# Kernel optimization log

Measured on AMD Instinct MI355X. Metric: run time of the kernel, lower is better.

The kernel has to match this reference:

```python
import jax, jax.numpy as jnp
import numpy as np

B, S_SRC, S_TRG = 128, 512, 128
VIN, VOUT = 128, 128
E, H = 128, 256          # embed, encoder hidden
HD = 2 * H               # decoder hidden = 512 (concat of bi-dir encoder states)
DENC = 2 * H             # encoder output feature dim = 512


def setup_inputs() -> dict:
    key = jax.random.key(0)
    ks = jax.random.split(key, 20)
    g = lambda k, shape: (jax.random.normal(k, shape, jnp.float32) * 0.05)
    inp = {
        "src": jax.random.randint(ks[0], (B, S_SRC), 0, VIN, jnp.int32),
        "trg": jax.random.randint(ks[1], (B, S_TRG), 0, VOUT, jnp.int32),
        # encoder
        "enc_emb": g(ks[2], (VIN, E)),
        "enc_Wih_f": g(ks[3], (4 * H, E)),
        "enc_Whh_f": g(ks[4], (4 * H, H)),
        "enc_b_f": g(ks[5], (4 * H,)),
        "enc_Wih_b": g(ks[6], (4 * H, E)),
        "enc_Whh_b": g(ks[7], (4 * H, H)),
        "enc_b_b": g(ks[8], (4 * H,)),
        # decoder
        "dec_emb": g(ks[9], (VOUT, E)),
        "dec_Wih": g(ks[10], (4 * HD, E + DENC)),
        "dec_Whh": g(ks[11], (4 * HD, HD)),
        "dec_b": g(ks[12], (4 * HD,)),
        # attention: Linear(dec_hid + enc_dim -> HD), v: Linear(HD -> 1)
        "attn_W": g(ks[13], (HD + DENC, HD)),
        "attn_b": g(ks[14], (HD,)),
        "attn_v": g(ks[15], (HD,)),
        # output projection
        "out_W": g(ks[16], (HD, VOUT)),
        "out_b": g(ks[17], (VOUT,)),
    }
    return inp


def _lstm_cell(h, c, x, Wih, Whh, b):
    gates = x @ Wih.T + h @ Whh.T + b               # [B, 4H]
    i, f, gg, o = jnp.split(gates, 4, axis=-1)       # PyTorch gate order i,f,g,o
    i, f, o = jax.nn.sigmoid(i), jax.nn.sigmoid(f), jax.nn.sigmoid(o)
    c = f * c + i * jnp.tanh(gg)
    h = o * jnp.tanh(c)
    return h, c


def _lstm_scan(xs, Wih, Whh, b, reverse=False):
    # xs: [S, B, E] -> hs: [S, B, H] (time-aligned), plus final (h, c)
    Bn, Hn = xs.shape[1], Whh.shape[1]
    init = (jnp.zeros((Bn, Hn), xs.dtype), jnp.zeros((Bn, Hn), xs.dtype))
    def step(carry, x):
        h, c = _lstm_cell(carry[0], carry[1], x, Wih, Whh, b)
        return (h, c), h
    (h, c), hs = jax.lax.scan(step, init, xs, reverse=reverse)
    return hs, h, c


def reference(src, trg, enc_emb, enc_Wih_f, enc_Whh_f, enc_b_f,
              enc_Wih_b, enc_Whh_b, enc_b_b, dec_emb, dec_Wih, dec_Whh,
              dec_b, attn_W, attn_b, attn_v, out_W, out_b):
    # ----- encoder (bidirectional LSTM) -----
    emb = enc_emb[src]                                # [B, S, E]
    xs = jnp.swapaxes(emb, 0, 1)                      # [S, B, E]
    hs_f, hf, cf = _lstm_scan(xs, enc_Wih_f, enc_Whh_f, enc_b_f, reverse=False)
    hs_b, hb, cb = _lstm_scan(xs, enc_Wih_b, enc_Whh_b, enc_b_b, reverse=True)
    enc_out = jnp.swapaxes(jnp.concatenate([hs_f, hs_b], -1), 0, 1)  # [B, S, 2H]
    hidden = jnp.concatenate([hf, hb], -1)            # [B, HD]  (hidden.view(1,B,-1))
    cell = jnp.concatenate([cf, cb], -1)              # [B, HD]

    # attention linear split: energy = tanh([h, enc] @ W + b)
    Wh, We = attn_W[:HD], attn_W[HD:]
    enc_proj = jnp.einsum("bsd,de->bse", enc_out, We)  # [B, S, HD] precomputed

    def dec_step(carry, tok):
        h, c = carry
        e = jnp.tanh(h[:, None, :] @ Wh + enc_proj + attn_b)     # [B, S, HD]
        scores = jnp.einsum("bse,e->bs", e, attn_v)              # [B, S]
        aw = jax.nn.softmax(scores, axis=1)
        ctx = jnp.einsum("bs,bsd->bd", aw, enc_out)              # [B, DENC]
        x = jnp.concatenate([dec_emb[tok], ctx], -1)             # [B, E+DENC]
        h, c = _lstm_cell(h, c, x, dec_Wih, dec_Whh, dec_b)
        logits = h @ out_W + out_b                               # [B, VOUT]
        return (h, c), logits

    # teacher forcing (ratio=1.0): input at step t is trg[:, t-1], t = 1..T-1
    toks = jnp.swapaxes(trg[:, :-1], 0, 1)            # [T-1, B]
    _, logits = jax.lax.scan(dec_step, (hidden, cell), toks)
    logits = jnp.swapaxes(logits, 0, 1)               # [B, T-1, VOUT]
    outputs = jnp.concatenate(
        [jnp.zeros((src.shape[0], 1, VOUT), logits.dtype), logits], axis=1)
    return outputs
```

## Files before the change

kernel.cpp:

```cpp
#include <hip/hip_runtime.h>


typedef _Float16 f16;
typedef _Float16 half8 __attribute__((ext_vector_type(8)));
typedef float f32x4 __attribute__((ext_vector_type(4)));
typedef char char8v __attribute__((ext_vector_type(8)));

#define MFMA16(a, b, c) __builtin_amdgcn_mfma_f32_16x16x32_f16((a), (b), (c), 0, 0, 0)

#define PSCALE (2.5f / 127.f)
#define PINV   (127.f / 2.5f)

__device__ __forceinline__ float fsig(float x) {
    return __builtin_amdgcn_rcpf(1.f + __expf(-x));
}
__device__ __forceinline__ float ftanh(float x) {
    return 1.f - 2.f * __builtin_amdgcn_rcpf(1.f + __expf(2.f * x));
}
__device__ __forceinline__ int frag_idx(int m, int k, int KS) {
    return (((m >> 4) * KS + (k >> 5)) * 64 + (((k >> 3) & 3) * 16 + (m & 15))) * 8 + (k & 7);
}

__device__ __forceinline__ void lds_barrier() {
    asm volatile("s_waitcnt lgkmcnt(0)" ::: "memory");
    __builtin_amdgcn_sched_barrier(0);
    __builtin_amdgcn_s_barrier();
    __builtin_amdgcn_sched_barrier(0);
}

__global__ void k_zero(unsigned* __restrict__ s)
{
    for (int z = threadIdx.x; z < 4112; z += 256) s[z] = 0u;
}

__global__ __launch_bounds__(256) void k_prep(
    const float* __restrict__ attn_W, const float* __restrict__ out_W,
    const float* __restrict__ enc_emb,
    const float* __restrict__ wihf, const float* __restrict__ wihb,
    const float* __restrict__ whhf, const float* __restrict__ whhb,
    const float* __restrict__ dec_emb, const float* __restrict__ dec_wih,
    const float* __restrict__ dec_whh,
    f16* __restrict__ WhT_sw, f16* __restrict__ outWT_sw,
    f16* __restrict__ whhf_sw, f16* __restrict__ whhb_sw,
    f16* __restrict__ decwih_sw, f16* __restrict__ decwhh_sw,
    f16* __restrict__ WeT, f16* __restrict__ emb16,
    f16* __restrict__ wihf16, f16* __restrict__ wihb16,
    f16* __restrict__ decemb16, float* __restrict__ out)
{
    long i = (long)blockIdx.x * 256 + threadIdx.x;
    if (i >= 3784704L) return;
    long idx = i;
    if (idx < 262144) {
        int j = idx & 7, lane = (idx >> 3) & 63, c = lane & 15, q = lane >> 4;
        int ks = (idx >> 9) & 15, nt = idx >> 13;
        WhT_sw[idx] = (f16)attn_W[(ks * 32 + q * 8 + j) * 512 + nt * 16 + c];
        return;
    }
    idx -= 262144;
    if (idx < 65536) {
        int j = idx & 7, lane = (idx >> 3) & 63, c = lane & 15, q = lane >> 4;
        int ks = (idx >> 9) & 15, nt = idx >> 13;
        outWT_sw[idx] = (f16)out_W[(ks * 32 + q * 8 + j) * 128 + nt * 16 + c];
        return;
    }
    idx -= 65536;
    if (idx < 262144) {
        int j = idx & 7, lane = (idx >> 3) & 63, c = lane & 15, q = lane >> 4;
        int ks = (idx >> 9) & 7, nt = idx >> 12;
        whhf_sw[idx] = (f16)whhf[(nt * 16 + c) * 256 + ks * 32 + q * 8 + j];
        return;
    }
    idx -= 262144;
    if (idx < 262144) {
        int j = idx & 7, lane = (idx >> 3) & 63, c = lane & 15, q = lane >> 4;
        int ks = (idx >> 9) & 7, nt = idx >> 12;
        whhb_sw[idx] = (f16)whhb[(nt * 16 + c) * 256 + ks * 32 + q * 8 + j];
        return;
    }
    idx -= 262144;
    if (idx < 1310720) {
        int j = idx & 7, lane = (idx >> 3) & 63, c = lane & 15, q = lane >> 4;
        int r2 = idx >> 9; int ks = r2 % 20, nt = r2 / 20;
        decwih_sw[idx] = (f16)dec_wih[(nt * 16 + c) * 640 + ks * 32 + q * 8 + j];
        return;
    }
    idx -= 1310720;
    if (idx < 1048576) {
        int j = idx & 7, lane = (idx >> 3) & 63, c = lane & 15, q = lane >> 4;
        int ks = (idx >> 9) & 15, nt = idx >> 13;
        decwhh_sw[idx] = (f16)dec_whh[(nt * 16 + c) * 512 + ks * 32 + q * 8 + j];
        return;
    }
    idx -= 1048576;
    if (idx < 262144) { int e = idx >> 9, d = idx & 511; WeT[idx] = (f16)attn_W[(512 + d) * 512 + e]; return; }
    idx -= 262144;
    if (idx < 16384)  { emb16[idx] = (f16)enc_emb[idx]; return; }
    idx -= 16384;
    if (idx < 131072) { wihf16[idx] = (f16)wihf[idx]; return; }
    idx -= 131072;
    if (idx < 131072) { wihb16[idx] = (f16)wihb[idx]; return; }
    idx -= 131072;
    if (idx < 16384)  { decemb16[idx] = (f16)dec_emb[idx]; return; }
    idx -= 16384;
    if (idx < 16384)  { int b = idx >> 7, v = idx & 127; out[b * 16384 + v] = 0.f; return; }
}

__global__ __launch_bounds__(256) void k_vocab(
    const f16* __restrict__ emb, const f16* __restrict__ wihf,
    const f16* __restrict__ wihb, const float* __restrict__ bf_,
    const float* __restrict__ bb_, f16* __restrict__ xg_vocab)
{
    int bn = blockIdx.x;
    int tid = threadIdx.x, wave = tid >> 6, lane = tid & 63;
    int col = lane & 15, quad = lane >> 4;
    int wr = wave >> 1, wc = wave & 1;

    f32x4 acc[4][4] = {};
    for (int ks = 0; ks < 4; ++ks) {
        int k0 = ks * 32 + quad * 8;
        half8 a[4], bfr[4];
        for (int i = 0; i < 4; ++i)
            a[i] = *(const half8*)(emb + (wr * 64 + i * 16 + col) * 128 + k0);
        for (int j = 0; j < 4; ++j) {
            int n = bn * 128 + wc * 64 + j * 16 + col;
            const f16* wp = (n < 1024) ? (wihf + n * 128) : (wihb + (n - 1024) * 128);
            bfr[j] = *(const half8*)(wp + k0);
        }
        for (int i = 0; i < 4; ++i)
            for (int j = 0; j < 4; ++j)
                acc[i][j] = MFMA16(a[i], bfr[j], acc[i][j]);
    }
    for (int j = 0; j < 4; ++j) {
        int n = bn * 128 + wc * 64 + j * 16 + col;
        float bias = (n < 1024) ? bf_[n] : bb_[n - 1024];
        for (int i = 0; i < 4; ++i) {
            int vbase = wr * 64 + i * 16 + quad * 4;
            for (int r = 0; r < 4; ++r)
                xg_vocab[(vbase + r) * 2048 + n] = (f16)(acc[i][j][r] + bias);
        }
    }
}

__global__ __launch_bounds__(512, 1) void k_enc(
    const int* __restrict__ src, const f16* __restrict__ xg_vocab,
    const f16* __restrict__ whhf_sw, const f16* __restrict__ whhb_sw,
    f16* __restrict__ enc_out, f16* __restrict__ hdec0, float* __restrict__ c_ws)
{
    int blk = blockIdx.x;
    int dir = blk >> 3, bbase = (blk & 7) * 16;
    int tid = threadIdx.x, wave = tid >> 6, lane = tid & 63;
    int col = lane & 15, quad = lane >> 4;
    const f16* whh = dir ? whhb_sw : whhf_sw;

    __shared__ f16 hb[2][16][264];
    __shared__ f16 xvb[2][16][1032];
    __shared__ unsigned short stall[8192];

    for (int z = tid; z < 2 * 16 * 264; z += 512) ((f16*)hb)[z] = (f16)0.f;
    for (int z = tid; z < 8192; z += 512) stall[z] = (unsigned short)src[bbase * 512 + z];
    float cc[2][4] = {};

    half8 bst[16];
    #pragma unroll
    for (int nt = 0; nt < 2; ++nt)
        #pragma unroll
        for (int kk = 0; kk < 8; ++kk) {
            int tile = wave * 2 + nt;
            bst[nt * 8 + kk] = *(const half8*)(whh + ((tile * 8 + kk) * 64 + lane) * 8);
        }
    __syncthreads();

    int xrow = tid >> 7, xoff = (tid & 127) * 8;
    half8 xr[4];
    {
        int ts0 = dir ? 511 : 0;
        #pragma unroll
        for (int it = 0; it < 4; ++it) {
            int row = it * 4 + xrow;
            int tok = stall[row * 512 + ts0];
            xr[it] = *(const half8*)(xg_vocab + tok * 2048 + dir * 1024 + xoff);
        }
        #pragma unroll
        for (int it = 0; it < 4; ++it)
            *(half8*)(&xvb[0][it * 4 + xrow][xoff]) = xr[it];
    }
    __syncthreads();

    int ts_prev = 0;
    for (int t = 0; t < 512; ++t) {
        int ts = dir ? (511 - t) : t;
        int cur = t & 1, prv = cur ^ 1;

        if (t < 511) {
            int tsn = dir ? (510 - t) : (t + 1);
            #pragma unroll
            for (int it = 0; it < 4; ++it) {
                int row = it * 4 + xrow;
                int tok = stall[row * 512 + tsn];
                xr[it] = *(const half8*)(xg_vocab + tok * 2048 + dir * 1024 + xoff);
            }
        }

        if (t > 0) {
            int b = tid >> 5, seg = tid & 31;
            *(half8*)(enc_out + ((size_t)(bbase + b) * 512 + ts_prev) * 512 + dir * 256 + seg * 8) =
                *(const half8*)(&hb[prv][b][seg * 8]);
        }

        half8 a[8];
        #pragma unroll
        for (int kk = 0; kk < 8; ++kk)
            a[kk] = *(const half8*)(&hb[prv][col][kk * 32 + quad * 8]);

        f32x4 acc[4][2] = {};
        #pragma unroll
        for (int kk = 0; kk < 8; ++kk) {
            half8 bv[6];
            #pragma unroll
            for (int g = 1; g < 4; ++g)
                #pragma unroll
                for (int nt = 0; nt < 2; ++nt) {
                    int tile = g * 16 + wave * 2 + nt;
                    bv[(g - 1) * 2 + nt] =
                        *(const half8*)(whh + ((tile * 8 + kk) * 64 + lane) * 8);
                }
            #pragma unroll
            for (int nt = 0; nt < 2; ++nt)
                acc[0][nt] = MFMA16(a[kk], bst[nt * 8 + kk], acc[0][nt]);
            #pragma unroll
            for (int g = 1; g < 4; ++g)
                #pragma unroll
                for (int nt = 0; nt < 2; ++nt)
                    acc[g][nt] = MFMA16(a[kk], bv[(g - 1) * 2 + nt], acc[g][nt]);
        }

        #pragma unroll
        for (int nt = 0; nt < 2; ++nt) {
            int hcol = wave * 32 + nt * 16 + col;
            #pragma unroll
            for (int r = 0; r < 4; ++r) {
                int b = quad * 4 + r;
                float gi = (float)xvb[cur][b][0 * 256 + hcol] + acc[0][nt][r];
                float gf = (float)xvb[cur][b][1 * 256 + hcol] + acc[1][nt][r];
                float gg = (float)xvb[cur][b][2 * 256 + hcol] + acc[2][nt][r];
                float go = (float)xvb[cur][b][3 * 256 + hcol] + acc[3][nt][r];
                float ig = fsig(gi), fg = fsig(gf), g2 = ftanh(gg), og = fsig(go);
                float cv = fg * cc[nt][r] + ig * g2;
                cc[nt][r] = cv;
                float h = og * ftanh(cv);
                hb[cur][b][hcol] = (f16)h;
            }
        }

        if (t < 511) {
            #pragma unroll
            for (int it = 0; it < 4; ++it)
                *(half8*)(&xvb[prv][it * 4 + xrow][xoff]) = xr[it];
        }

        lds_barrier();
        ts_prev = ts;
    }

    {
        int b = tid >> 5, seg = tid & 31;
        *(half8*)(enc_out + ((size_t)(bbase + b) * 512 + ts_prev) * 512 + dir * 256 + seg * 8) =
            *(const half8*)(&hb[1][b][seg * 8]);
    }
    #pragma unroll
    for (int nt = 0; nt < 2; ++nt) {
        int hcol = wave * 32 + nt * 16 + col;
        #pragma unroll
        for (int r = 0; r < 4; ++r) {
            int b = quad * 4 + r;
            int m = bbase + b, k = dir * 256 + hcol;
            hdec0[frag_idx(m, k, 16)] = hb[1][b][hcol];
            c_ws[m * 512 + k] = cc[nt][r];
        }
    }
}

__global__ __launch_bounds__(256) void k_proj(
    const f16* __restrict__ enc_out, const f16* __restrict__ WeT,
    char* __restrict__ proj8)
{
    int blk = blockIdx.x;
    int bm = blk & 511, bn = blk >> 9;
    int tid = threadIdx.x, wave = tid >> 6, lane = tid & 63;
    int col = lane & 15, quad = lane >> 4;
    int wr = wave >> 1, wc = wave & 1;

    f32x4 acc[4][4] = {};
    for (int ks = 0; ks < 16; ++ks) {
        int k0 = ks * 32 + quad * 8;
        half8 a[4], bfr[4];
        for (int i = 0; i < 4; ++i) {
            int m = bm * 128 + wr * 64 + i * 16 + col;
            a[i] = *(const half8*)(enc_out + (size_t)m * 512 + k0);
        }
        for (int j = 0; j < 4; ++j) {
            int n = bn * 128 + wc * 64 + j * 16 + col;
            bfr[j] = *(const half8*)(WeT + n * 512 + k0);
        }
        for (int i = 0; i < 4; ++i)
            for (int j = 0; j < 4; ++j)
                acc[i][j] = MFMA16(a[i], bfr[j], acc[i][j]);
    }
    for (int j = 0; j < 4; ++j) {
        int n = bn * 128 + wc * 64 + j * 16 + col;
        for (int i = 0; i < 4; ++i) {
            int mbase = bm * 128 + wr * 64 + i * 16 + quad * 4;
            for (int r = 0; r < 4; ++r) {
                float v = acc[i][j][r] * PINV;
                int q = (int)rintf(v);
                q = (q > 127) ? 127 : ((q < -127) ? -127 : q);
                proj8[(size_t)(mbase + r) * 512 + n] = (char)q;
            }
        }
    }
}

__global__ __launch_bounds__(256) void k_qinit(
    const f16* __restrict__ h0_sw, const f16* __restrict__ WhT_sw,
    float* __restrict__ qpart)
{
    int j = blockIdx.x;
    int tid = threadIdx.x, wave = tid >> 6, lane = tid & 63;
    int col = lane & 15, quad = lane >> 4;
    half8 a[2];
    #pragma unroll
    for (int i = 0; i < 2; ++i)
        a[i] = *(const half8*)(h0_sw + (((wave * 2 + i) * 16 + j) * 64 + lane) * 8);
    for (int nt = 0; nt < 32; ++nt) {
        half8 bfr = *(const half8*)(WhT_sw + ((nt * 16 + j) * 64 + lane) * 8);
        f32x4 q0 = {}, q1 = {};
        q0 = MFMA16(a[0], bfr, q0);
        q1 = MFMA16(a[1], bfr, q1);
        #pragma unroll
        for (int r = 0; r < 4; ++r) {
            qpart[(j * 128 + wave * 32 + quad * 4 + r) * 512 + nt * 16 + col] = q0[r];
            qpart[(j * 128 + wave * 32 + 16 + quad * 4 + r) * 512 + nt * 16 + col] = q1[r];
        }
    }
}

__global__ __launch_bounds__(512, 4) void k_step(
    const char* __restrict__ proj8, const f16* __restrict__ enc_out,
    float* __restrict__ qpart, const float* __restrict__ attn_bp,
    const float* __restrict__ attn_vp, const int* __restrict__ trg,
    const f16* __restrict__ dec_emb, f16* __restrict__ x_sw,
    float* __restrict__ part_m, float* __restrict__ part_l,
    float* __restrict__ part_ctx, f16* __restrict__ hdec0,
    f16* __restrict__ hdec1, const f16* __restrict__ wih_sw,
    const f16* __restrict__ whh_sw, const float* __restrict__ dec_bp,
    float* __restrict__ c_ws, f16* __restrict__ hhist_sw,
    const f16* __restrict__ WhT_sw, unsigned* __restrict__ flags, int tt)
{
    int blk = blockIdx.x;
    int tid = threadIdx.x, wave = tid >> 6, lane = tid & 63;
    int col = lane & 15, quad = lane >> 4;

    __shared__ float q[512];
    __shared__ float sc[256];
    __shared__ float ctxred[8][512];
    __shared__ float wred[8], wred2[8];
    __shared__ f16 hsl[64][40];
    __shared__ float gm[64][2];
    __shared__ int islast;

    if (blk < 32) {
        int tg = tt - 1;
        if (tg >= 0) {
            int j = blk >> 1, mh = blk & 1;
            if (tid < 64) {
                int bb = mh * 64 + tid;
                float m0 = part_m[bb * 2 + 0], m1 = part_m[bb * 2 + 1];
                float l0 = part_l[bb * 2 + 0], l1 = part_l[bb * 2 + 1];
                float M = fmaxf(m0, m1);
                float g0 = __expf(m0 - M), g1 = __expf(m1 - M);
                float inv = 1.f / (g0 * l0 + g1 * l1);
                gm[tid][0] = g0 * inv;
                gm[tid][1] = g1 * inv;
            }
            __syncthreads();
            for (int z = tid; z < 32768; z += 512) {
                int lr = z >> 9, d = z & 511;
                int bb = mh * 64 + lr;
                float c = gm[lr][0] * part_ctx[(size_t)(bb * 2 + 0) * 512 + d]
                        + gm[lr][1] * part_ctx[(size_t)(bb * 2 + 1) * 512 + d];
                x_sw[frag_idx(bb, 128 + d, 20)] = (f16)c;
            }
            __syncthreads();

            if (tid < 256) {
                const f16* hprev = (tg & 1) ? hdec1 : hdec0;
                f16* hnext = (tg & 1) ? hdec0 : hdec1;

                f32x4 acc[8] = {};
                for (int ks = 0; ks < 36; ++ks) {
                    int mtile = mh * 4 + wave;
                    half8 a = (ks < 20)
                        ? *(const half8*)(x_sw + ((mtile * 20 + ks) * 64 + lane) * 8)
                        : *(const half8*)(hprev + ((mtile * 16 + (ks - 20)) * 64 + lane) * 8);
                    half8 bv[8];
                    #pragma unroll
                    for (int jt = 0; jt < 8; ++jt) {
                        int g = jt >> 1, u2 = jt & 1;
                        int ntile = g * 32 + j * 2 + u2;
                        bv[jt] = (ks < 20)
                            ? *(const half8*)(wih_sw + ((ntile * 20 + ks) * 64 + lane) * 8)
                            : *(const half8*)(whh_sw + ((ntile * 16 + (ks - 20)) * 64 + lane) * 8);
                    }
                    #pragma unroll
                    for (int jt = 0; jt < 8; ++jt)
                        acc[jt] = MFMA16(a, bv[jt], acc[jt]);
                }
                float bias[8];
                #pragma unroll
                for (int jt = 0; jt < 8; ++jt) {
                    int g = jt >> 1, u2 = jt & 1;
                    bias[jt] = dec_bp[g * 512 + j * 32 + u2 * 16 + col];
                }
                #pragma unroll
                for (int r = 0; r < 4; ++r) {
                    int lb = wave * 16 + quad * 4 + r;
                    int bb = mh * 64 + lb;
                    #pragma unroll
                    for (int u2 = 0; u2 < 2; ++u2) {
                        int hl = u2 * 16 + col, hcol = j * 32 + hl;
                        float gi = acc[0 + u2][r] + bias[0 + u2];
                        float gf = acc[2 + u2][r] + bias[2 + u2];
                        float gg = acc[4 + u2][r] + bias[4 + u2];
                        float go = acc[6 + u2][r] + bias[6 + u2];
                        float ig = fsig(gi), fg = fsig(gf), g2 = ftanh(gg), og = fsig(go);
                        float cv = fg * c_ws[bb * 512 + hcol] + ig * g2;
                        c_ws[bb * 512 + hcol] = cv;
                        float h = og * ftanh(cv);
                        f16 h16 = (f16)h;
                        int fidx = frag_idx(bb, hcol, 16);
                        hnext[fidx] = h16;
                        hhist_sw[tg * 65536 + fidx] = h16;
                        hsl[lb][hl] = h16;
                    }
                }
                half8 aq = *(const half8*)(&hsl[wave * 16 + col][quad * 8]);
                for (int nt = 0; nt < 32; ++nt) {
                    half8 bq = *(const half8*)(WhT_sw + ((nt * 16 + j) * 64 + lane) * 8);
                    f32x4 q0 = {};
                    q0 = MFMA16(aq, bq, q0);
                    #pragma unroll
                    for (int r = 0; r < 4; ++r)
                        qpart[(j * 128 + mh * 64 + wave * 16 + quad * 4 + r) * 512 + nt * 16 + col] = q0[r];
                }
            }

            __syncthreads();
            if (tid == 0) {
                unsigned old = __hip_atomic_fetch_add(flags, 1u, __ATOMIC_ACQ_REL,
                                                      __HIP_MEMORY_SCOPE_AGENT);
                islast = (old == (unsigned)(32 * tt - 1)) ? 1 : 0;
            }
            __syncthreads();
            if (islast && tid < 256)
                __hip_atomic_store(flags + 16 + tid * 16, (unsigned)tt,
                                   __ATOMIC_RELEASE, __HIP_MEMORY_SCOPE_AGENT);
        }
        return;
    }

    int ab = blk - 32;
    int b = ab >> 1, sh = ab & 1;
    int sbase = sh * 256;

    float vreg[8];
    #pragma unroll
    for (int u = 0; u < 8; ++u) vreg[u] = attn_vp[lane * 8 + u];
    float abias = attn_bp[tid];

    if (tt > 0) {
        if (tid == 0) {
            while (__hip_atomic_load(flags + 16 + ab * 16, __ATOMIC_RELAXED,
                                     __HIP_MEMORY_SCOPE_AGENT) < (unsigned)tt)
                __builtin_amdgcn_s_sleep(16);
            (void)__hip_atomic_load(flags + 16 + ab * 16, __ATOMIC_ACQUIRE,
                                    __HIP_MEMORY_SCOPE_AGENT);
        }
        __syncthreads();
    }

    {
        float s = abias;
        #pragma unroll
        for (int jj = 0; jj < 16; ++jj) s += qpart[(jj * 128 + b) * 512 + tid];
        q[tid] = s;
    }
    __syncthreads();

    float qreg[8];
    #pragma unroll
    for (int u = 0; u < 8; ++u) qreg[u] = q[lane * 8 + u];

    for (int ib = 0; ib < 4; ++ib) {
        char8v p[8];
        #pragma unroll
        for (int z = 0; z < 8; ++z) {
            int sl = (ib * 8 + z) * 8 + wave;
            p[z] = *(const char8v*)(proj8 + ((size_t)b * 512 + sbase + sl) * 512 + lane * 8);
        }
        #pragma unroll
        for (int z = 0; z < 8; ++z) {
            int sl = (ib * 8 + z) * 8 + wave;
            float part = 0.f;
            #pragma unroll
            for (int u = 0; u < 8; ++u)
                part += vreg[u] * ftanh(fmaf((float)p[z][u], PSCALE, qreg[u]));
            #pragma unroll
            for (int o = 32; o; o >>= 1) part += __shfl_xor(part, o);
            if (lane == 0) sc[sl] = part;
        }
    }
    __syncthreads();

    float s0 = (tid < 256) ? sc[tid] : -__builtin_inff();
    float mv = s0;
    #pragma unroll
    for (int o = 32; o; o >>= 1) mv = fmaxf(mv, __shfl_xor(mv, o));
    if (lane == 0) wred[wave] = mv;
    __syncthreads();
    float M = wred[0];
    #pragma unroll
    for (int w = 1; w < 8; ++w) M = fmaxf(M, wred[w]);
    float e0 = (tid < 256) ? __expf(s0 - M) : 0.f;
    if (tid < 256) sc[tid] = e0;
    float sm = e0;
    #pragma unroll
    for (int o = 32; o; o >>= 1) sm += __shfl_xor(sm, o);
    if (lane == 0) wred2[wave] = sm;
    __syncthreads();
    float lsum = wred2[0];
    #pragma unroll
    for (int w = 1; w < 8; ++w) lsum += wred2[w];

    float a8[8] = {};
    for (int ib = 0; ib < 4; ++ib) {
        half8 ev[8];
        float wgt[8];
        #pragma unroll
        for (int z = 0; z < 8; ++z) {
            int sl = (ib * 8 + z) * 8 + wave;
            ev[z] = *(const half8*)(enc_out + ((size_t)b * 512 + sbase + sl) * 512 + lane * 8);
            wgt[z] = sc[sl];
        }
        #pragma unroll
        for (int z = 0; z < 8; ++z)
            #pragma unroll
            for (int u = 0; u < 8; ++u) a8[u] += wgt[z] * (float)ev[z][u];
    }
    #pragma unroll
    for (int u = 0; u < 8; ++u) ctxred[wave][lane * 8 + u] = a8[u];
    __syncthreads();
    float cp = 0.f;
    #pragma unroll
    for (int w = 0; w < 8; ++w) cp += ctxred[w][tid];
    part_ctx[(size_t)ab * 512 + tid] = cp;
    if (tid == 0) { part_m[ab] = M; part_l[ab] = lsum; }

    if (sh == 0 && tid < 128) {
        int tok = trg[b * 128 + tt];
        x_sw[frag_idx(b, tid, 20)] = dec_emb[tok * 128 + tid];
    }
}

__global__ __launch_bounds__(256) void k_gates(
    f16* __restrict__ x_sw, const f16* __restrict__ hprev_sw,
    const f16* __restrict__ wih_sw, const f16* __restrict__ whh_sw,
    const float* __restrict__ dec_b, float* __restrict__ c_ws,
    f16* __restrict__ hnext_sw, f16* __restrict__ hhist_sw,
    const f16* __restrict__ WhT_sw, float* __restrict__ qpart,
    const float* __restrict__ part_m, const float* __restrict__ part_l,
    const float* __restrict__ part_ctx, int t)
{
    int jb = blockIdx.x;
    int j = jb >> 1, mh = jb & 1;
    int tid = threadIdx.x, wave = tid >> 6, lane = tid & 63;
    int col = lane & 15, quad = lane >> 4;
    __shared__ f16 hsl[64][40];
    __shared__ float gm[64][2];

    if (tid < 64) {
        int bb = mh * 64 + tid;
        float m0 = part_m[bb * 2 + 0], m1 = part_m[bb * 2 + 1];
        float l0 = part_l[bb * 2 + 0], l1 = part_l[bb * 2 + 1];
        float M = fmaxf(m0, m1);
        float g0 = __expf(m0 - M), g1 = __expf(m1 - M);
        float inv = 1.f / (g0 * l0 + g1 * l1);
        gm[tid][0] = g0 * inv;
        gm[tid][1] = g1 * inv;
    }
    __syncthreads();
    for (int z = tid; z < 32768; z += 256) {
        int lr = z >> 9, d = z & 511;
        int bb = mh * 64 + lr;
        float c = gm[lr][0] * part_ctx[(size_t)(bb * 2 + 0) * 512 + d]
                + gm[lr][1] * part_ctx[(size_t)(bb * 2 + 1) * 512 + d];
        x_sw[frag_idx(bb, 128 + d, 20)] = (f16)c;
    }
    __syncthreads();

    f32x4 acc[8] = {};
    for (int ks = 0; ks < 36; ++ks) {
        int mtile = mh * 4 + wave;
        half8 a = (ks < 20)
            ? *(const half8*)(x_sw + ((mtile * 20 + ks) * 64 + lane) * 8)
            : *(const half8*)(hprev_sw + ((mtile * 16 + (ks - 20)) * 64 + lane) * 8);
        half8 bv[8];
        #pragma unroll
        for (int jt = 0; jt < 8; ++jt) {
            int g = jt >> 1, u2 = jt & 1;
            int ntile = g * 32 + j * 2 + u2;
            bv[jt] = (ks < 20)
                ? *(const half8*)(wih_sw + ((ntile * 20 + ks) * 64 + lane) * 8)
                : *(const half8*)(whh_sw + ((ntile * 16 + (ks - 20)) * 64 + lane) * 8);
        }
        #pragma unroll
        for (int jt = 0; jt < 8; ++jt)
            acc[jt] = MFMA16(a, bv[jt], acc[jt]);
    }
    float bias[8];
    #pragma unroll
    for (int jt = 0; jt < 8; ++jt) {
        int g = jt >> 1, u2 = jt & 1;
        bias[jt] = dec_b[g * 512 + j * 32 + u2 * 16 + col];
    }
    #pragma unroll
    for (int r = 0; r < 4; ++r) {
        int lb = wave * 16 + quad * 4 + r;
        int bb = mh * 64 + lb;
        #pragma unroll
        for (int u2 = 0; u2 < 2; ++u2) {
            int hl = u2 * 16 + col, hcol = j * 32 + hl;
            float gi = acc[0 + u2][r] + bias[0 + u2];
            float gf = acc[2 + u2][r] + bias[2 + u2];
            float gg = acc[4 + u2][r] + bias[4 + u2];
            float go = acc[6 + u2][r] + bias[6 + u2];
            float ig = fsig(gi), fg = fsig(gf), g2 = ftanh(gg), og = fsig(go);
            float cv = fg * c_ws[bb * 512 + hcol] + ig * g2;
            c_ws[bb * 512 + hcol] = cv;
            float h = og * ftanh(cv);
            f16 h16 = (f16)h;
            int fidx = frag_idx(bb, hcol, 16);
            hnext_sw[fidx] = h16;
            hhist_sw[t * 65536 + fidx] = h16;
            hsl[lb][hl] = h16;
        }
    }
    half8 aq = *(const half8*)(&hsl[wave * 16 + col][quad * 8]);
    for (int nt = 0; nt < 32; ++nt) {
        half8 bq = *(const half8*)(WhT_sw + ((nt * 16 + j) * 64 + lane) * 8);
        f32x4 q0 = {};
        q0 = MFMA16(aq, bq, q0);
        #pragma unroll
        for (int r = 0; r < 4; ++r)
            qpart[(j * 128 + mh * 64 + wave * 16 + quad * 4 + r) * 512 + nt * 16 + col] = q0[r];
    }
}

__global__ __launch_bounds__(256) void k_logits(
    const f16* __restrict__ hhist_sw, const f16* __restrict__ outWT_sw,
    const float* __restrict__ out_b, float* __restrict__ out)
{
    int bt = blockIdx.x;
    int tid = threadIdx.x, wave = tid >> 6, lane = tid & 63;
    int col = lane & 15, quad = lane >> 4;
    f32x4 acc[2][8] = {};
    for (int ks = 0; ks < 16; ++ks) {
        half8 a[2];
        #pragma unroll
        for (int i = 0; i < 2; ++i)
            a[i] = *(const half8*)(hhist_sw + bt * 65536 + (((wave * 2 + i) * 16 + ks) * 64 + lane) * 8);
        half8 bv[8];
        #pragma unroll
        for (int jt = 0; jt < 8; ++jt)
            bv[jt] = *(const half8*)(outWT_sw + ((jt * 16 + ks) * 64 + lane) * 8);
        #pragma unroll
        for (int jt = 0; jt < 8; ++jt) {
            acc[0][jt] = MFMA16(a[0], bv[jt], acc[0][jt]);
            acc[1][jt] = MFMA16(a[1], bv[jt], acc[1][jt]);
        }
    }
    #pragma unroll
    for (int jt = 0; jt < 8; ++jt) {
        float bias = out_b[jt * 16 + col];
        #pragma unroll
        for (int i = 0; i < 2; ++i)
            #pragma unroll
            for (int r = 0; r < 4; ++r) {
                int br = wave * 32 + i * 16 + quad * 4 + r;
                out[br * 16384 + (bt + 1) * 128 + jt * 16 + col] = acc[i][jt][r] + bias;
            }
    }
}

extern "C" void kernel_launch(void* const* d_in, const int* in_sizes, int n_in,
                              void* d_out, int out_size, void* d_ws, size_t ws_size,
                              hipStream_t stream)
{
    (void)in_sizes; (void)n_in; (void)out_size;
    if (ws_size < 130000000) return;

    const int*   src     = (const int*)d_in[0];
    const int*   trg     = (const int*)d_in[1];
    const float* enc_emb = (const float*)d_in[2];
    const float* wihf    = (const float*)d_in[3];
    const float* whhf    = (const float*)d_in[4];
    const float* bf_     = (const float*)d_in[5];
    const float* wihb    = (const float*)d_in[6];
    const float* whhb    = (const float*)d_in[7];
    const float* bb_     = (const float*)d_in[8];
    const float* dec_emb = (const float*)d_in[9];
    const float* dec_wih = (const float*)d_in[10];
    const float* dec_whh = (const float*)d_in[11];
    const float* dec_b   = (const float*)d_in[12];
    const float* attn_W  = (const float*)d_in[13];
    const float* attn_b  = (const float*)d_in[14];
    const float* attn_v  = (const float*)d_in[15];
    const float* out_W   = (const float*)d_in[16];
    const float* out_b   = (const float*)d_in[17];
    float* out = (float*)d_out;

    char* p = (char*)d_ws;
    auto carve = [&](size_t n) { char* r = p; p += ((n + 255) & ~(size_t)255); return r; };
    f16*   enc_out   = (f16*)  carve(67108864);
    char*  proj8     = (char*) carve(33554432);
    f16*   WhT_sw    = (f16*)  carve(524288);
    f16*   WeT       = (f16*)  carve(524288);
    f16*   outWT_sw  = (f16*)  carve(131072);
    f16*   emb16     = (f16*)  carve(32768);
    f16*   wihf16    = (f16*)  carve(262144);
    f16*   wihb16    = (f16*)  carve(262144);
    f16*   whhf_sw   = (f16*)  carve(524288);
    f16*   whhb_sw   = (f16*)  carve(524288);
    f16*   decemb16  = (f16*)  carve(32768);
    f16*   decwih_sw = (f16*)  carve(2621440);
    f16*   decwhh_sw = (f16*)  carve(2097152);
    float* qpart     = (float*)carve(4194304);
    f16*   hdec0     = (f16*)  carve(131072);
    f16*   hdec1     = (f16*)  carve(131072);
    float* c_ws      = (float*)carve(262144);
    f16*   x_sw      = (f16*)  carve(163840);
    f16*   hhist_sw  = (f16*)  carve(16646144);
    f16*   xg_vocab  = (f16*)  carve(524288);
    float* part_m    = (float*)carve(2048);
    float* part_l    = (float*)carve(2048);
    float* part_ctx  = (float*)carve(524288);
    unsigned* flagsv = (unsigned*)carve(16448);

    k_zero<<<1, 256, 0, stream>>>(flagsv);
    k_prep<<<14784, 256, 0, stream>>>(attn_W, out_W, enc_emb, wihf, wihb, whhf, whhb,
                                      dec_emb, dec_wih, dec_whh,
                                      WhT_sw, outWT_sw, whhf_sw, whhb_sw,
                                      decwih_sw, decwhh_sw, WeT, emb16,
                                      wihf16, wihb16, decemb16, out);
    k_vocab<<<16, 256, 0, stream>>>(emb16, wihf16, wihb16, bf_, bb_, xg_vocab);
    k_enc<<<16, 512, 0, stream>>>(src, xg_vocab, whhf_sw, whhb_sw, enc_out, hdec0, c_ws);
    k_proj<<<2048, 256, 0, stream>>>(enc_out, WeT, proj8);
    k_qinit<<<16, 256, 0, stream>>>(hdec0, WhT_sw, qpart);

    for (int tt = 0; tt < 127; ++tt)
        k_step<<<288, 512, 0, stream>>>(proj8, enc_out, qpart, attn_b, attn_v,
                                        trg, decemb16, x_sw, part_m, part_l,
                                        part_ctx, hdec0, hdec1, decwih_sw,
                                        decwhh_sw, dec_b, c_ws, hhist_sw,
                                        WhT_sw, flagsv, tt);
    k_gates<<<32, 256, 0, stream>>>(x_sw, hdec0, decwih_sw, decwhh_sw, dec_b,
                                    c_ws, hdec1, hhist_sw, WhT_sw, qpart,
                                    part_m, part_l, part_ctx, 126);

    k_logits<<<127, 256, 0, stream>>>(hhist_sw, outWT_sw, out_b, out);
}
```

Baseline: 12.46 ms.

## Use one 1024-thread attention block per batch row, dropping split-softmax merge

Attention blocks now cover all 512 source positions of one batch row with 1024 threads, instead of two 512-thread blocks each covering half the sequence. The full softmax and context are finished inside one block and written straight into x_sw. This removes the partial max/sum/context buffers and the merge pass the gate blocks used to run before their GEMM. The final gates kernel is cut down to skip the unused q projection and hidden write. In exchange there are half as many attention blocks, each with more threads and shared memory, so occupancy and per-step latency may shift.

```diff
diff --git a/kernel.cpp b/kernel.cpp
--- a/kernel.cpp
+++ b/kernel.cpp
@@ -344,54 +344,32 @@
     }
 }
 
-__global__ __launch_bounds__(512, 4) void k_step(
+__global__ __launch_bounds__(1024, 4) void k_step(
     const char* __restrict__ proj8, const f16* __restrict__ enc_out,
     float* __restrict__ qpart, const float* __restrict__ attn_bp,
     const float* __restrict__ attn_vp, const int* __restrict__ trg,
     const f16* __restrict__ dec_emb, f16* __restrict__ x_sw,
-    float* __restrict__ part_m, float* __restrict__ part_l,
-    float* __restrict__ part_ctx, f16* __restrict__ hdec0,
-    f16* __restrict__ hdec1, const f16* __restrict__ wih_sw,
-    const f16* __restrict__ whh_sw, const float* __restrict__ dec_bp,
-    float* __restrict__ c_ws, f16* __restrict__ hhist_sw,
-    const f16* __restrict__ WhT_sw, unsigned* __restrict__ flags, int tt)
+    f16* __restrict__ hdec0, f16* __restrict__ hdec1,
+    const f16* __restrict__ wih_sw, const f16* __restrict__ whh_sw,
+    const float* __restrict__ dec_bp, float* __restrict__ c_ws,
+    f16* __restrict__ hhist_sw, const f16* __restrict__ WhT_sw,
+    unsigned* __restrict__ flags, int tt)
 {
     int blk = blockIdx.x;
     int tid = threadIdx.x, wave = tid >> 6, lane = tid & 63;
     int col = lane & 15, quad = lane >> 4;
 
     __shared__ float q[512];
-    __shared__ float sc[256];
-    __shared__ float ctxred[8][512];
-    __shared__ float wred[8], wred2[8];
+    __shared__ float sc[512];
+    __shared__ float ctxred[16][512];
+    __shared__ float wred[16], wred2[16];
     __shared__ f16 hsl[64][40];
-    __shared__ float gm[64][2];
     __shared__ int islast;
 
     if (blk < 32) {
         int tg = tt - 1;
         if (tg >= 0) {
             int j = blk >> 1, mh = blk & 1;
-            if (tid < 64) {
-                int bb = mh * 64 + tid;
-                float m0 = part_m[bb * 2 + 0], m1 = part_m[bb * 2 + 1];
-                float l0 = part_l[bb * 2 + 0], l1 = part_l[bb * 2 + 1];
-                float M = fmaxf(m0, m1);
-                float g0 = __expf(m0 - M), g1 = __expf(m1 - M);
-                float inv = 1.f / (g0 * l0 + g1 * l1);
-                gm[tid][0] = g0 * inv;
-                gm[tid][1] = g1 * inv;
-            }
-            __syncthreads();
-            for (int z = tid; z < 32768; z += 512) {
-                int lr = z >> 9, d = z & 511;
-                int bb = mh * 64 + lr;
-                float c = gm[lr][0] * part_ctx[(size_t)(bb * 2 + 0) * 512 + d]
-                        + gm[lr][1] * part_ctx[(size_t)(bb * 2 + 1) * 512 + d];
-                x_sw[frag_idx(bb, 128 + d, 20)] = (f16)c;
-            }
-            __syncthreads();
-
             if (tid < 256) {
                 const f16* hprev = (tg & 1) ? hdec1 : hdec0;
                 f16* hnext = (tg & 1) ? hdec0 : hdec1;
@@ -461,35 +439,32 @@
                 islast = (old == (unsigned)(32 * tt - 1)) ? 1 : 0;
             }
             __syncthreads();
-            if (islast && tid < 256)
+            if (islast && tid < 128)
                 __hip_atomic_store(flags + 16 + tid * 16, (unsigned)tt,
                                    __ATOMIC_RELEASE, __HIP_MEMORY_SCOPE_AGENT);
         }
         return;
     }
 
-    int ab = blk - 32;
-    int b = ab >> 1, sh = ab & 1;
-    int sbase = sh * 256;
+    int b = blk - 32;
 
     float vreg[8];
     #pragma unroll
     for (int u = 0; u < 8; ++u) vreg[u] = attn_vp[lane * 8 + u];
-    float abias = attn_bp[tid];
 
     if (tt > 0) {
         if (tid == 0) {
-            while (__hip_atomic_load(flags + 16 + ab * 16, __ATOMIC_RELAXED,
+            while (__hip_atomic_load(flags + 16 + b * 16, __ATOMIC_RELAXED,
                                      __HIP_MEMORY_SCOPE_AGENT) < (unsigned)tt)
                 __builtin_amdgcn_s_sleep(16);
-            (void)__hip_atomic_load(flags + 16 + ab * 16, __ATOMIC_ACQUIRE,
+            (void)__hip_atomic_load(flags + 16 + b * 16, __ATOMIC_ACQUIRE,
                                     __HIP_MEMORY_SCOPE_AGENT);
         }
         __syncthreads();
     }
 
-    {
-        float s = abias;
+    if (tid < 512) {
+        float s = attn_bp[tid];
         #pragma unroll
         for (int jj = 0; jj < 16; ++jj) s += qpart[(jj * 128 + b) * 512 + tid];
         q[tid] = s;
@@ -504,12 +479,12 @@
         char8v p[8];
         #pragma unroll
         for (int z = 0; z < 8; ++z) {
-            int sl = (ib * 8 + z) * 8 + wave;
-            p[z] = *(const char8v*)(proj8 + ((size_t)b * 512 + sbase + sl) * 512 + lane * 8);
+            int sl = (ib * 8 + z) * 16 + wave;
+            p[z] = *(const char8v*)(proj8 + ((size_t)b * 512 + sl) * 512 + lane * 8);
         }
         #pragma unroll
         for (int z = 0; z < 8; ++z) {
-            int sl = (ib * 8 + z) * 8 + wave;
+            int sl = (ib * 8 + z) * 16 + wave;
             float part = 0.f;
             #pragma unroll
             for (int u = 0; u < 8; ++u)
@@ -521,7 +496,7 @@
     }
     __syncthreads();
 
-    float s0 = (tid < 256) ? sc[tid] : -__builtin_inff();
+    float s0 = (tid < 512) ? sc[tid] : -__builtin_inff();
     float mv = s0;
     #pragma unroll
     for (int o = 32; o; o >>= 1) mv = fmaxf(mv, __shfl_xor(mv, o));
@@ -529,9 +504,9 @@
     __syncthreads();
     float M = wred[0];
     #pragma unroll
-    for (int w = 1; w < 8; ++w) M = fmaxf(M, wred[w]);
-    float e0 = (tid < 256) ? __expf(s0 - M) : 0.f;
-    if (tid < 256) sc[tid] = e0;
+    for (int w = 1; w < 16; ++w) M = fmaxf(M, wred[w]);
+    float e0 = (tid < 512) ? __expf(s0 - M) : 0.f;
+    if (tid < 512) sc[tid] = e0;
     float sm = e0;
     #pragma unroll
     for (int o = 32; o; o >>= 1) sm += __shfl_xor(sm, o);
@@ -539,7 +514,7 @@
     __syncthreads();
     float lsum = wred2[0];
     #pragma unroll
-    for (int w = 1; w < 8; ++w) lsum += wred2[w];
+    for (int w = 1; w < 16; ++w) lsum += wred2[w];
 
     float a8[8] = {};
     for (int ib = 0; ib < 4; ++ib) {
@@ -547,8 +522,8 @@
         float wgt[8];
         #pragma unroll
         for (int z = 0; z < 8; ++z) {
-            int sl = (ib * 8 + z) * 8 + wave;
-            ev[z] = *(const half8*)(enc_out + ((size_t)b * 512 + sbase + sl) * 512 + lane * 8);
+            int sl = (ib * 8 + z) * 16 + wave;
+            ev[z] = *(const half8*)(enc_out + ((size_t)b * 512 + sl) * 512 + lane * 8);
             wgt[z] = sc[sl];
         }
         #pragma unroll
@@ -559,53 +534,28 @@
     #pragma unroll
     for (int u = 0; u < 8; ++u) ctxred[wave][lane * 8 + u] = a8[u];
     __syncthreads();
-    float cp = 0.f;
-    #pragma unroll
-    for (int w = 0; w < 8; ++w) cp += ctxred[w][tid];
-    part_ctx[(size_t)ab * 512 + tid] = cp;
-    if (tid == 0) { part_m[ab] = M; part_l[ab] = lsum; }
-
-    if (sh == 0 && tid < 128) {
+    if (tid < 512) {
+        float cp = 0.f;
+        #pragma unroll
+        for (int w = 0; w < 16; ++w) cp += ctxred[w][tid];
+        x_sw[frag_idx(b, 128 + tid, 20)] = (f16)(cp * (1.f / lsum));
+    }
+    if (tid < 128) {
         int tok = trg[b * 128 + tt];
         x_sw[frag_idx(b, tid, 20)] = dec_emb[tok * 128 + tid];
     }
 }
 
-__global__ __launch_bounds__(256) void k_gates(
-    f16* __restrict__ x_sw, const f16* __restrict__ hprev_sw,
+__global__ __launch_bounds__(256) void k_gates_fin(
+    const f16* __restrict__ x_sw, const f16* __restrict__ hprev_sw,
     const f16* __restrict__ wih_sw, const f16* __restrict__ whh_sw,
     const float* __restrict__ dec_b, float* __restrict__ c_ws,
-    f16* __restrict__ hnext_sw, f16* __restrict__ hhist_sw,
-    const f16* __restrict__ WhT_sw, float* __restrict__ qpart,
-    const float* __restrict__ part_m, const float* __restrict__ part_l,
-    const float* __restrict__ part_ctx, int t)
+    f16* __restrict__ hhist_sw, int t)
 {
     int jb = blockIdx.x;
     int j = jb >> 1, mh = jb & 1;
     int tid = threadIdx.x, wave = tid >> 6, lane = tid & 63;
     int col = lane & 15, quad = lane >> 4;
-    __shared__ f16 hsl[64][40];
-    __shared__ float gm[64][2];
-
-    if (tid < 64) {
-        int bb = mh * 64 + tid;
-        float m0 = part_m[bb * 2 + 0], m1 = part_m[bb * 2 + 1];
-        float l0 = part_l[bb * 2 + 0], l1 = part_l[bb * 2 + 1];
-        float M = fmaxf(m0, m1);
-        float g0 = __expf(m0 - M), g1 = __expf(m1 - M);
-        float inv = 1.f / (g0 * l0 + g1 * l1);
-        gm[tid][0] = g0 * inv;
-        gm[tid][1] = g1 * inv;
-    }
-    __syncthreads();
-    for (int z = tid; z < 32768; z += 256) {
-        int lr = z >> 9, d = z & 511;
-        int bb = mh * 64 + lr;
-        float c = gm[lr][0] * part_ctx[(size_t)(bb * 2 + 0) * 512 + d]
-                + gm[lr][1] * part_ctx[(size_t)(bb * 2 + 1) * 512 + d];
-        x_sw[frag_idx(bb, 128 + d, 20)] = (f16)c;
-    }
-    __syncthreads();
 
     f32x4 acc[8] = {};
     for (int ks = 0; ks < 36; ++ks) {
@@ -647,21 +597,8 @@
             float cv = fg * c_ws[bb * 512 + hcol] + ig * g2;
             c_ws[bb * 512 + hcol] = cv;
             float h = og * ftanh(cv);
-            f16 h16 = (f16)h;
-            int fidx = frag_idx(bb, hcol, 16);
-            hnext_sw[fidx] = h16;
-            hhist_sw[t * 65536 + fidx] = h16;
-            hsl[lb][hl] = h16;
-        }
-    }
-    half8 aq = *(const half8*)(&hsl[wave * 16 + col][quad * 8]);
-    for (int nt = 0; nt < 32; ++nt) {
-        half8 bq = *(const half8*)(WhT_sw + ((nt * 16 + j) * 64 + lane) * 8);
-        f32x4 q0 = {};
-        q0 = MFMA16(aq, bq, q0);
-        #pragma unroll
-        for (int r = 0; r < 4; ++r)
-            qpart[(j * 128 + mh * 64 + wave * 16 + quad * 4 + r) * 512 + nt * 16 + col] = q0[r];
+            hhist_sw[t * 65536 + frag_idx(bb, hcol, 16)] = (f16)h;
+        }
     }
 }
 
@@ -750,9 +687,6 @@
     f16*   x_sw      = (f16*)  carve(163840);
     f16*   hhist_sw  = (f16*)  carve(16646144);
     f16*   xg_vocab  = (f16*)  carve(524288);
-    float* part_m    = (float*)carve(2048);
-    float* part_l    = (float*)carve(2048);
-    float* part_ctx  = (float*)carve(524288);
     unsigned* flagsv = (unsigned*)carve(16448);
 
     k_zero<<<1, 256, 0, stream>>>(flagsv);
@@ -767,14 +701,12 @@
     k_qinit<<<16, 256, 0, stream>>>(hdec0, WhT_sw, qpart);
 
     for (int tt = 0; tt < 127; ++tt)
-        k_step<<<288, 512, 0, stream>>>(proj8, enc_out, qpart, attn_b, attn_v,
-                                        trg, decemb16, x_sw, part_m, part_l,
-                                        part_ctx, hdec0, hdec1, decwih_sw,
-                                        decwhh_sw, dec_b, c_ws, hhist_sw,
-                                        WhT_sw, flagsv, tt);
-    k_gates<<<32, 256, 0, stream>>>(x_sw, hdec0, decwih_sw, decwhh_sw, dec_b,
-                                    c_ws, hdec1, hhist_sw, WhT_sw, qpart,
-                                    part_m, part_l, part_ctx, 126);
+        k_step<<<160, 1024, 0, stream>>>(proj8, enc_out, qpart, attn_b, attn_v,
+                                         trg, decemb16, x_sw, hdec0, hdec1,
+                                         decwih_sw, decwhh_sw, dec_b, c_ws,
+                                         hhist_sw, WhT_sw, flagsv, tt);
+    k_gates_fin<<<32, 256, 0, stream>>>(x_sw, hdec0, decwih_sw, decwhh_sw,
+                                        dec_b, c_ws, hhist_sw, 126);
 
     k_logits<<<127, 256, 0, stream>>>(hhist_sw, outWT_sw, out_b, out);
 }
```

Result: slower. 12.89 ms (+3.5%).

## Replace counter-based grid barrier with per-producer flags and prefetch projection before wait

Applied to the files above, without the earlier changes.

Producer blocks no longer increment a shared atomic counter and have the last one broadcast flags to all consumers. Each producer now publishes its own per-block flag, and consumer blocks poll all 32 flags with one wave and check them with a ballot. This removes the serialized fetch-add and the extra broadcast hop. The first chunk of the int8 projection is also loaded before the wait so the load latency overlaps the spin. Consumers now issue more polling traffic (32 loads per poll per block), and the prefetch adds register pressure.

```diff
diff --git a/kernel.cpp b/kernel.cpp
--- a/kernel.cpp
+++ b/kernel.cpp
@@ -366,7 +366,6 @@
     __shared__ float wred[8], wred2[8];
     __shared__ f16 hsl[64][40];
     __shared__ float gm[64][2];
-    __shared__ int islast;
 
     if (blk < 32) {
         int tg = tt - 1;
@@ -455,14 +454,8 @@
             }
 
             __syncthreads();
-            if (tid == 0) {
-                unsigned old = __hip_atomic_fetch_add(flags, 1u, __ATOMIC_ACQ_REL,
-                                                      __HIP_MEMORY_SCOPE_AGENT);
-                islast = (old == (unsigned)(32 * tt - 1)) ? 1 : 0;
-            }
-            __syncthreads();
-            if (islast && tid < 256)
-                __hip_atomic_store(flags + 16 + tid * 16, (unsigned)tt,
+            if (tid == 0)
+                __hip_atomic_store(flags + blk * 16, (unsigned)tt,
                                    __ATOMIC_RELEASE, __HIP_MEMORY_SCOPE_AGENT);
         }
         return;
@@ -477,13 +470,26 @@
     for (int u = 0; u < 8; ++u) vreg[u] = attn_vp[lane * 8 + u];
     float abias = attn_bp[tid];
 
+    char8v p0[8];
+    #pragma unroll
+    for (int z = 0; z < 8; ++z) {
+        int sl = z * 8 + wave;
+        p0[z] = *(const char8v*)(proj8 + ((size_t)b * 512 + sbase + sl) * 512 + lane * 8);
+    }
+
     if (tt > 0) {
-        if (tid == 0) {
-            while (__hip_atomic_load(flags + 16 + ab * 16, __ATOMIC_RELAXED,
-                                     __HIP_MEMORY_SCOPE_AGENT) < (unsigned)tt)
-                __builtin_amdgcn_s_sleep(16);
-            (void)__hip_atomic_load(flags + 16 + ab * 16, __ATOMIC_ACQUIRE,
-                                    __HIP_MEMORY_SCOPE_AGENT);
+        if (wave == 0) {
+            for (;;) {
+                unsigned v = (lane < 32)
+                    ? __hip_atomic_load(flags + lane * 16, __ATOMIC_RELAXED,
+                                        __HIP_MEMORY_SCOPE_AGENT)
+                    : (unsigned)tt;
+                if (__ballot(v >= (unsigned)tt) == ~0ull) break;
+                __builtin_amdgcn_s_sleep(8);
+            }
+            if (lane == 0)
+                (void)__hip_atomic_load(flags, __ATOMIC_ACQUIRE,
+                                        __HIP_MEMORY_SCOPE_AGENT);
         }
         __syncthreads();
     }
@@ -500,7 +506,18 @@
     #pragma unroll
     for (int u = 0; u < 8; ++u) qreg[u] = q[lane * 8 + u];
 
-    for (int ib = 0; ib < 4; ++ib) {
+    #pragma unroll
+    for (int z = 0; z < 8; ++z) {
+        int sl = z * 8 + wave;
+        float part = 0.f;
+        #pragma unroll
+        for (int u = 0; u < 8; ++u)
+            part += vreg[u] * ftanh(fmaf((float)p0[z][u], PSCALE, qreg[u]));
+        #pragma unroll
+        for (int o = 32; o; o >>= 1) part += __shfl_xor(part, o);
+        if (lane == 0) sc[sl] = part;
+    }
+    for (int ib = 1; ib < 4; ++ib) {
         char8v p[8];
         #pragma unroll
         for (int z = 0; z < 8; ++z) {
```

Result: no change. 12.52 ms (+0.4%).
